# Kernel tuning notes

Measured on AMD Instinct MI355X. Metric: run time of the kernel, lower is better.

The kernel has to match this reference:

```python
import jax, jax.numpy as jnp
import numpy as np

NUM_HEADS = 4
KEY_DIM = 8
WINDOW = 4
SHIFT = 2
CHANNELS = 32


def setup_inputs() -> dict:
    key = jax.random.key(0)
    ks = jax.random.split(key, 9)
    C, H, D = CHANNELS, NUM_HEADS, KEY_DIM
    s = 0.05
    return {
        "x": jax.random.normal(ks[0], (4, 512, 512, C), jnp.float32),
        "Wq": jax.random.normal(ks[1], (C, H, D), jnp.float32) * s,
        "bq": jax.random.normal(ks[2], (H, D), jnp.float32) * s,
        "Wk": jax.random.normal(ks[3], (C, H, D), jnp.float32) * s,
        "bk": jax.random.normal(ks[4], (H, D), jnp.float32) * s,
        "Wv": jax.random.normal(ks[5], (C, H, D), jnp.float32) * s,
        "bv": jax.random.normal(ks[6], (H, D), jnp.float32) * s,
        "Wo": jax.random.normal(ks[7], (H, D, C), jnp.float32) * s,
        "bo": jax.random.normal(ks[8], (C,), jnp.float32) * s,
    }


def reference(x, Wq, bq, Wk, bk, Wv, bv, Wo, bo):
    B, H, W, C = x.shape
    ws, sh = WINDOW, SHIFT
    pad_h = (ws - H % ws) % ws
    pad_w = (ws - W % ws) % ws
    p = jnp.pad(x, ((0, 0), (0, pad_h), (0, pad_w), (0, 0)))
    if sh:
        p = jnp.roll(p, shift=(-sh, -sh), axis=(1, 2))
    Hp, Wp = H + pad_h, W + pad_w
    hw, ww = Hp // ws, Wp // ws
    # partition into windows: [B*hw*ww, ws*ws, C]
    win = p.reshape(B, hw, ws, ww, ws, C).transpose(0, 1, 3, 2, 4, 5)
    win = win.reshape(-1, ws * ws, C)
    # multi-head self-attention within each window (Keras MultiHeadAttention math)
    q = jnp.einsum('bnc,chd->bnhd', win, Wq) + bq
    k = jnp.einsum('bnc,chd->bnhd', win, Wk) + bk
    v = jnp.einsum('bnc,chd->bnhd', win, Wv) + bv
    scores = jnp.einsum('bqhd,bkhd->bhqk', q, k) / np.sqrt(KEY_DIM).astype(np.float32)
    attn = jax.nn.softmax(scores, axis=-1)
    o = jnp.einsum('bhqk,bkhd->bqhd', attn, v)
    out = jnp.einsum('bqhd,hdc->bqc', o, Wo) + bo
    # merge windows back: [B, Hp, Wp, C]
    out = out.reshape(B, hw, ww, ws, ws, C).transpose(0, 1, 3, 2, 4, 5)
    out = out.reshape(B, Hp, Wp, C)
    if sh:
        out = jnp.roll(out, shift=(sh, sh), axis=(1, 2))
    out = out[:, :H, :W, :]
    return x + out
```

## Files before the change

kernel.cpp:

```cpp
#include <hip/hip_runtime.h>
#include <hip/hip_bf16.h>
#include <stdint.h>

typedef float f32x4 __attribute__((ext_vector_type(4)));
typedef short s16x8 __attribute__((ext_vector_type(8)));
typedef unsigned short u16;
typedef u16 u16x4 __attribute__((ext_vector_type(4)));

__device__ __forceinline__ u16 f2bf(float f) {
    union { __hip_bfloat16 h; u16 u; } cv;
    cv.h = __float2bfloat16(f);
    return cv.u;
}
__device__ __forceinline__ f32x4 mfma16(s16x8 a, s16x8 b, f32x4 c) {
    return __builtin_amdgcn_mfma_f32_16x16x32_bf16(a, b, c, 0, 0, 0);
}
__device__ __forceinline__ float exp2_hw(float x) {
    float r; asm("v_exp_f32 %0, %1" : "=v"(r) : "v"(x)); return r;
}
#define LDS_FENCE() asm volatile("s_waitcnt lgkmcnt(0)" ::: "memory")

__global__ __launch_bounds__(256) void swin_attn_kernel(
    const float* __restrict__ x,
    const float* __restrict__ Wq, const float* __restrict__ bq,
    const float* __restrict__ Wk, const float* __restrict__ bk,
    const float* __restrict__ Wv, const float* __restrict__ bv,
    const float* __restrict__ Wo, const float* __restrict__ bo,
    float* __restrict__ out)
{
    const int lane  = threadIdx.x & 63;
    const int wave  = threadIdx.x >> 6;
    const int col16 = lane & 15;
    const int g     = lane >> 4;

    __shared__ __align__(16) u16 qk_bf[4][16][72];
    __shared__ __align__(16) u16 vT_bf[4][32][24];
    __shared__ __align__(16) u16 p_bf[4][4][16][24];
    __shared__ __align__(16) u16 o_bf[4][16][40];

    const float scale  = 0.35355339059327373f;
    const float qscale = scale * 1.4426950408889634f;

    s16x8 wqkv[6];
    #pragma unroll
    for (int j = 0; j < 6; ++j) {
        const float* Wsrc = (j < 2) ? Wq : (j < 4) ? Wk : Wv;
        const int colW = ((j & 1) << 4) | col16;
        const float sc = (j < 2) ? qscale : 1.0f;
        s16x8 wf;
        #pragma unroll
        for (int jj = 0; jj < 8; ++jj)
            wf[jj] = (short)f2bf(Wsrc[(g * 8 + jj) * 32 + colW] * sc);
        wqkv[j] = wf;
    }
    f32x4 bias_qk[4];
    #pragma unroll
    for (int j = 0; j < 4; ++j) {
        const float* bsrc = (j < 2) ? bq : bk;
        const float sc = (j < 2) ? qscale : 1.0f;
        #pragma unroll
        for (int i = 0; i < 4; ++i)
            bias_qk[j][i] = bsrc[((j & 1) << 4) + 4 * g + i] * sc;
    }
    f32x4 bias_v[2];
    #pragma unroll
    for (int jv = 0; jv < 2; ++jv) {
        float b = bv[jv * 16 + col16];
        bias_v[jv] = (f32x4){b, b, b, b};
    }
    s16x8 wo_frag[2];
    f32x4 bo_frag[2];
    #pragma unroll
    for (int j2 = 0; j2 < 2; ++j2) {
        const int cout = j2 * 16 + col16;
        s16x8 wf;
        #pragma unroll
        for (int jj = 0; jj < 8; ++jj)
            wf[jj] = (short)f2bf(Wo[(g * 8 + jj) * 32 + cout]);
        wo_frag[j2] = wf;
        #pragma unroll
        for (int i = 0; i < 4; ++i)
            bo_frag[j2][i] = bo[j2 * 16 + 4 * g + i];
    }

    const f32x4 zero4 = {0.f, 0.f, 0.f, 0.f};
    const s16x8 zero8 = {0, 0, 0, 0, 0, 0, 0, 0};

    const int wbase = (blockIdx.x * 4 + wave) * 4;
    long curpix;
    f32x4 px0, px1;
    {
        const int w = wbase;
        const int b = w >> 14, rem = w & 16383, wi = rem >> 7, wj = rem & 127;
        const int row  = (wi * 4 + (col16 >> 2) + 2) & 511;
        const int colp = (wj * 4 + (col16 & 3) + 2) & 511;
        curpix = ((((long)b << 9) + row) * 512 + colp) * 32;
        px0 = *(const f32x4*)(x + curpix + g * 8);
        px1 = *(const f32x4*)(x + curpix + g * 8 + 4);
    }

    #pragma unroll 1
    for (int it = 0; it < 4; ++it) {
        s16x8 xfrag;
        #pragma unroll
        for (int i = 0; i < 4; ++i) {
            xfrag[i]     = (short)f2bf(px0[i]);
            xfrag[i + 4] = (short)f2bf(px1[i]);
        }
        const long pixbase = curpix;

        #pragma unroll
        for (int j = 0; j < 4; ++j) {
            f32x4 c = mfma16(wqkv[j], xfrag, bias_qk[j]);
            u16x4 qv;
            #pragma unroll
            for (int i = 0; i < 4; ++i) qv[i] = f2bf(c[i]);
            *(u16x4*)&qk_bf[wave][col16][j * 16 + 4 * g] = qv;
        }
        #pragma unroll
        for (int jv = 0; jv < 2; ++jv) {
            f32x4 c = mfma16(xfrag, wqkv[4 + jv], bias_v[jv]);
            u16x4 vv;
            #pragma unroll
            for (int i = 0; i < 4; ++i) vv[i] = f2bf(c[i]);
            *(u16x4*)&vT_bf[wave][jv * 16 + col16][4 * g] = vv;
        }

        {
            const int w = wbase + ((it + 1) & 3);
            const int b = w >> 14, rem = w & 16383, wi = rem >> 7, wj = rem & 127;
            const int row  = (wi * 4 + (col16 >> 2) + 2) & 511;
            const int colp = (wj * 4 + (col16 & 3) + 2) & 511;
            const long np = ((((long)b << 9) + row) * 512 + colp) * 32;
            px0 = *(const f32x4*)(x + np + g * 8);
            px1 = *(const f32x4*)(x + np + g * 8 + 4);
            curpix = np;
        }
        f32x4 r0 = *(const f32x4*)(x + pixbase + 4 * g);
        f32x4 r1 = *(const f32x4*)(x + pixbase + 16 + 4 * g);

        LDS_FENCE();

        f32x4 s[4];
        #pragma unroll
        for (int h = 0; h < 4; ++h) {
            s16x8 afrag = zero8, bfrag = zero8;
            if (g == 0) {
                afrag = *(const s16x8*)&qk_bf[wave][col16][32 + h * 8];
                bfrag = *(const s16x8*)&qk_bf[wave][col16][h * 8];
            }
            s[h] = mfma16(afrag, bfrag, zero4);
        }
        #pragma unroll
        for (int h = 0; h < 4; ++h) {
            float p0 = exp2_hw(s[h][0]);
            float p1 = exp2_hw(s[h][1]);
            float p2 = exp2_hw(s[h][2]);
            float p3 = exp2_hw(s[h][3]);
            float sum = (p0 + p1) + (p2 + p3);
            sum += __shfl_xor(sum, 16);
            sum += __shfl_xor(sum, 32);
            const float inv = __builtin_amdgcn_rcpf(sum);
            u16x4 pv;
            pv[0] = f2bf(p0 * inv); pv[1] = f2bf(p1 * inv);
            pv[2] = f2bf(p2 * inv); pv[3] = f2bf(p3 * inv);
            *(u16x4*)&p_bf[wave][h][col16][4 * g] = pv;
        }
        LDS_FENCE();

        #pragma unroll
        for (int h = 0; h < 4; ++h) {
            s16x8 vfrag = zero8, pfrag = zero8;
            if (g < 2) {
                vfrag = *(const s16x8*)&vT_bf[wave][h * 8 + (col16 & 7)][g * 8];
                pfrag = *(const s16x8*)&p_bf[wave][h][col16][g * 8];
            }
            f32x4 oc = mfma16(vfrag, pfrag, zero4);
            if (g < 2) {
                u16x4 ov;
                #pragma unroll
                for (int i = 0; i < 4; ++i) ov[i] = f2bf(oc[i]);
                *(u16x4*)&o_bf[wave][col16][h * 8 + 4 * g] = ov;
            }
        }
        LDS_FENCE();

        s16x8 ofrag = *(const s16x8*)&o_bf[wave][col16][g * 8];
        {
            f32x4 c = mfma16(wo_frag[0], ofrag, bo_frag[0]);
            #pragma unroll
            for (int i = 0; i < 4; ++i) c[i] += r0[i];
            *(f32x4*)(out + pixbase + 4 * g) = c;
        }
        {
            f32x4 c = mfma16(wo_frag[1], ofrag, bo_frag[1]);
            #pragma unroll
            for (int i = 0; i < 4; ++i) c[i] += r1[i];
            *(f32x4*)(out + pixbase + 16 + 4 * g) = c;
        }
    }
}

extern "C" void kernel_launch(void* const* d_in, const int* in_sizes, int n_in,
                              void* d_out, int out_size, void* d_ws, size_t ws_size,
                              hipStream_t stream) {
    const float* x  = (const float*)d_in[0];
    const float* Wq = (const float*)d_in[1];
    const float* bq = (const float*)d_in[2];
    const float* Wk = (const float*)d_in[3];
    const float* bk = (const float*)d_in[4];
    const float* Wv = (const float*)d_in[5];
    const float* bv = (const float*)d_in[6];
    const float* Wo = (const float*)d_in[7];
    const float* bo = (const float*)d_in[8];
    float* out = (float*)d_out;

    dim3 grid(4096), block(256);
    hipLaunchKernelGGL(swin_attn_kernel, grid, block, 0, stream,
                       x, Wq, bq, Wk, bk, Wv, bv, Wo, bo, out);
}
```

Before: 64.65 us.

## Keep attention fragments in registers using 32x32 MFMA and cross-lane permutes

Removes all LDS staging of Q/K/V, probabilities and outputs. Fragments are now exchanged through permlane32_swap and ds_swizzle, and head pairs are batched into 32x32x16 MFMAs with weight layouts permuted to match. The aim is to remove the LDS round-trips and waitcnt stalls between stages. In exchange it adds block-diagonal masking work, more register pressure, and a launch-bounds occupancy hint.

```diff
diff --git a/kernel.cpp b/kernel.cpp
--- a/kernel.cpp
+++ b/kernel.cpp
@@ -3,24 +3,46 @@
 #include <stdint.h>
 
 typedef float f32x4 __attribute__((ext_vector_type(4)));
+typedef float f32x16 __attribute__((ext_vector_type(16)));
 typedef short s16x8 __attribute__((ext_vector_type(8)));
 typedef unsigned short u16;
-typedef u16 u16x4 __attribute__((ext_vector_type(4)));
 
 __device__ __forceinline__ u16 f2bf(float f) {
     union { __hip_bfloat16 h; u16 u; } cv;
     cv.h = __float2bfloat16(f);
     return cv.u;
 }
+__device__ __forceinline__ int pkbf(float lo, float hi) {
+    return (int)(unsigned)f2bf(lo) | ((int)(unsigned)f2bf(hi) << 16);
+}
 __device__ __forceinline__ f32x4 mfma16(s16x8 a, s16x8 b, f32x4 c) {
     return __builtin_amdgcn_mfma_f32_16x16x32_bf16(a, b, c, 0, 0, 0);
 }
+__device__ __forceinline__ f32x16 mfma32(s16x8 a, s16x8 b, f32x16 c) {
+    return __builtin_amdgcn_mfma_f32_32x32x16_bf16(a, b, c, 0, 0, 0);
+}
 __device__ __forceinline__ float exp2_hw(float x) {
     float r; asm("v_exp_f32 %0, %1" : "=v"(r) : "v"(x)); return r;
 }
-#define LDS_FENCE() asm volatile("s_waitcnt lgkmcnt(0)" ::: "memory")
-
-__global__ __launch_bounds__(256) void swin_attn_kernel(
+__device__ __forceinline__ int swz16(int v) {
+    return __builtin_amdgcn_ds_swizzle(v, 0x401F);
+}
+__device__ __forceinline__ int pl_hi_to_lo(int v) {
+    auto r = __builtin_amdgcn_permlane32_swap(v, v, false, false);
+    return r[1];
+}
+__device__ __forceinline__ void pl_pair(int a, int b, int* xo, int* yo) {
+    auto r = __builtin_amdgcn_permlane32_swap(a, b, false, false);
+    *xo = r[0];
+    *yo = r[1];
+}
+__device__ __forceinline__ s16x8 frag4(int d0, int d1, int d2, int d3) {
+    union { int i[4]; s16x8 v; } u;
+    u.i[0] = d0; u.i[1] = d1; u.i[2] = d2; u.i[3] = d3;
+    return u.v;
+}
+
+__global__ __launch_bounds__(256, 3) void swin_attn_kernel(
     const float* __restrict__ x,
     const float* __restrict__ Wq, const float* __restrict__ bq,
     const float* __restrict__ Wk, const float* __restrict__ bk,
@@ -28,30 +50,36 @@
     const float* __restrict__ Wo, const float* __restrict__ bo,
     float* __restrict__ out)
 {
-    const int lane  = threadIdx.x & 63;
-    const int wave  = threadIdx.x >> 6;
-    const int col16 = lane & 15;
-    const int g     = lane >> 4;
-
-    __shared__ __align__(16) u16 qk_bf[4][16][72];
-    __shared__ __align__(16) u16 vT_bf[4][32][24];
-    __shared__ __align__(16) u16 p_bf[4][4][16][24];
-    __shared__ __align__(16) u16 o_bf[4][16][40];
-
-    const float scale  = 0.35355339059327373f;
-    const float qscale = scale * 1.4426950408889634f;
+    const int lane = threadIdx.x & 63;
+    const int wave = threadIdx.x >> 6;
+    const int c16  = lane & 15;
+    const int g    = lane >> 4;
+    const int hc   = g & 1;
+    const bool lo32  = (lane < 32);
+    const bool rowok = (hc == 0);
+
+    const float qscale = 0.35355339059327373f * 1.4426950408889634f;
 
     s16x8 wqkv[6];
     #pragma unroll
-    for (int j = 0; j < 6; ++j) {
-        const float* Wsrc = (j < 2) ? Wq : (j < 4) ? Wk : Wv;
-        const int colW = ((j & 1) << 4) | col16;
+    for (int j = 0; j < 4; ++j) {
+        const float* Wsrc = (j < 2) ? Wq : Wk;
         const float sc = (j < 2) ? qscale : 1.0f;
+        const int h = c16 >> 2, d = (j & 1) * 4 + (c16 & 3);
         s16x8 wf;
         #pragma unroll
         for (int jj = 0; jj < 8; ++jj)
-            wf[jj] = (short)f2bf(Wsrc[(g * 8 + jj) * 32 + colW] * sc);
+            wf[jj] = (short)f2bf(Wsrc[(g * 8 + jj) * 32 + h * 8 + d] * sc);
         wqkv[j] = wf;
+    }
+    #pragma unroll
+    for (int jv = 0; jv < 2; ++jv) {
+        const int h = jv * 2 + (c16 >> 3), d = c16 & 7;
+        s16x8 wf;
+        #pragma unroll
+        for (int jj = 0; jj < 8; ++jj)
+            wf[jj] = (short)f2bf(Wv[(g * 8 + jj) * 32 + h * 8 + d]);
+        wqkv[4 + jv] = wf;
     }
     f32x4 bias_qk[4];
     #pragma unroll
@@ -60,31 +88,56 @@
         const float sc = (j < 2) ? qscale : 1.0f;
         #pragma unroll
         for (int i = 0; i < 4; ++i)
-            bias_qk[j][i] = bsrc[((j & 1) << 4) + 4 * g + i] * sc;
+            bias_qk[j][i] = bsrc[g * 8 + (j & 1) * 4 + i] * sc;
     }
     f32x4 bias_v[2];
     #pragma unroll
     for (int jv = 0; jv < 2; ++jv) {
-        float b = bv[jv * 16 + col16];
+        float b = bv[(jv * 2 + (c16 >> 3)) * 8 + (c16 & 7)];
         bias_v[jv] = (f32x4){b, b, b, b};
     }
     s16x8 wo_frag[2];
     f32x4 bo_frag[2];
     #pragma unroll
     for (int j2 = 0; j2 < 2; ++j2) {
-        const int cout = j2 * 16 + col16;
+        const int cout = j2 * 16 + c16;
         s16x8 wf;
         #pragma unroll
-        for (int jj = 0; jj < 8; ++jj)
-            wf[jj] = (short)f2bf(Wo[(g * 8 + jj) * 32 + cout]);
+        for (int jj = 0; jj < 8; ++jj) {
+            const int h = (g & 1) + 2 * (jj >> 2);
+            const int d = 4 * (g >> 1) + (jj & 3);
+            wf[jj] = (short)f2bf(Wo[(h * 8 + d) * 32 + cout]);
+        }
         wo_frag[j2] = wf;
         #pragma unroll
         for (int i = 0; i < 4; ++i)
             bo_frag[j2][i] = bo[j2 * 16 + 4 * g + i];
     }
 
-    const f32x4 zero4 = {0.f, 0.f, 0.f, 0.f};
-    const s16x8 zero8 = {0, 0, 0, 0, 0, 0, 0, 0};
+    f32x16 zero16;
+    #pragma unroll
+    for (int i = 0; i < 16; ++i) zero16[i] = 0.0f;
+
+    auto softmax_pack = [&](const f32x16& S) -> s16x8 {
+        float e[8];
+        #pragma unroll
+        for (int i = 0; i < 8; ++i) {
+            float sv = hc ? S[8 + i] : S[i];
+            e[i] = exp2_hw(sv);
+        }
+        float s = ((e[0] + e[1]) + (e[2] + e[3])) + ((e[4] + e[5]) + (e[6] + e[7]));
+        auto rs = __builtin_amdgcn_permlane32_swap(__float_as_int(s), __float_as_int(s), false, false);
+        float partner = lo32 ? __int_as_float(rs[1]) : __int_as_float(rs[0]);
+        float inv = __builtin_amdgcn_rcpf(s + partner);
+        #pragma unroll
+        for (int i = 0; i < 8; ++i) e[i] *= inv;
+        int dw0 = pkbf(e[0], e[1]), dw1 = pkbf(e[2], e[3]);
+        int dw2 = pkbf(e[4], e[5]), dw3 = pkbf(e[6], e[7]);
+        int a0, b0, a1, b1;
+        pl_pair(dw0, dw2, &a0, &b0);
+        pl_pair(dw1, dw3, &a1, &b1);
+        return frag4(a0, a1, b0, b1);
+    };
 
     const int wbase = (blockIdx.x * 4 + wave) * 4;
     long curpix;
@@ -92,8 +145,8 @@
     {
         const int w = wbase;
         const int b = w >> 14, rem = w & 16383, wi = rem >> 7, wj = rem & 127;
-        const int row  = (wi * 4 + (col16 >> 2) + 2) & 511;
-        const int colp = (wj * 4 + (col16 & 3) + 2) & 511;
+        const int row  = (wi * 4 + (c16 >> 2) + 2) & 511;
+        const int colp = (wj * 4 + (c16 & 3) + 2) & 511;
         curpix = ((((long)b << 9) + row) * 512 + colp) * 32;
         px0 = *(const f32x4*)(x + curpix + g * 8);
         px1 = *(const f32x4*)(x + curpix + g * 8 + 4);
@@ -101,36 +154,15 @@
 
     #pragma unroll 1
     for (int it = 0; it < 4; ++it) {
-        s16x8 xfrag;
-        #pragma unroll
-        for (int i = 0; i < 4; ++i) {
-            xfrag[i]     = (short)f2bf(px0[i]);
-            xfrag[i + 4] = (short)f2bf(px1[i]);
-        }
         const long pixbase = curpix;
-
-        #pragma unroll
-        for (int j = 0; j < 4; ++j) {
-            f32x4 c = mfma16(wqkv[j], xfrag, bias_qk[j]);
-            u16x4 qv;
-            #pragma unroll
-            for (int i = 0; i < 4; ++i) qv[i] = f2bf(c[i]);
-            *(u16x4*)&qk_bf[wave][col16][j * 16 + 4 * g] = qv;
-        }
-        #pragma unroll
-        for (int jv = 0; jv < 2; ++jv) {
-            f32x4 c = mfma16(xfrag, wqkv[4 + jv], bias_v[jv]);
-            u16x4 vv;
-            #pragma unroll
-            for (int i = 0; i < 4; ++i) vv[i] = f2bf(c[i]);
-            *(u16x4*)&vT_bf[wave][jv * 16 + col16][4 * g] = vv;
-        }
+        s16x8 xfrag = frag4(pkbf(px0[0], px0[1]), pkbf(px0[2], px0[3]),
+                            pkbf(px1[0], px1[1]), pkbf(px1[2], px1[3]));
 
         {
             const int w = wbase + ((it + 1) & 3);
             const int b = w >> 14, rem = w & 16383, wi = rem >> 7, wj = rem & 127;
-            const int row  = (wi * 4 + (col16 >> 2) + 2) & 511;
-            const int colp = (wj * 4 + (col16 & 3) + 2) & 511;
+            const int row  = (wi * 4 + (c16 >> 2) + 2) & 511;
+            const int colp = (wj * 4 + (c16 & 3) + 2) & 511;
             const long np = ((((long)b << 9) + row) * 512 + colp) * 32;
             px0 = *(const f32x4*)(x + np + g * 8);
             px1 = *(const f32x4*)(x + np + g * 8 + 4);
@@ -139,65 +171,61 @@
         f32x4 r0 = *(const f32x4*)(x + pixbase + 4 * g);
         f32x4 r1 = *(const f32x4*)(x + pixbase + 16 + 4 * g);
 
-        LDS_FENCE();
-
-        f32x4 s[4];
-        #pragma unroll
-        for (int h = 0; h < 4; ++h) {
-            s16x8 afrag = zero8, bfrag = zero8;
-            if (g == 0) {
-                afrag = *(const s16x8*)&qk_bf[wave][col16][32 + h * 8];
-                bfrag = *(const s16x8*)&qk_bf[wave][col16][h * 8];
-            }
-            s[h] = mfma16(afrag, bfrag, zero4);
-        }
-        #pragma unroll
-        for (int h = 0; h < 4; ++h) {
-            float p0 = exp2_hw(s[h][0]);
-            float p1 = exp2_hw(s[h][1]);
-            float p2 = exp2_hw(s[h][2]);
-            float p3 = exp2_hw(s[h][3]);
-            float sum = (p0 + p1) + (p2 + p3);
-            sum += __shfl_xor(sum, 16);
-            sum += __shfl_xor(sum, 32);
-            const float inv = __builtin_amdgcn_rcpf(sum);
-            u16x4 pv;
-            pv[0] = f2bf(p0 * inv); pv[1] = f2bf(p1 * inv);
-            pv[2] = f2bf(p2 * inv); pv[3] = f2bf(p3 * inv);
-            *(u16x4*)&p_bf[wave][h][col16][4 * g] = pv;
-        }
-        LDS_FENCE();
-
-        #pragma unroll
-        for (int h = 0; h < 4; ++h) {
-            s16x8 vfrag = zero8, pfrag = zero8;
-            if (g < 2) {
-                vfrag = *(const s16x8*)&vT_bf[wave][h * 8 + (col16 & 7)][g * 8];
-                pfrag = *(const s16x8*)&p_bf[wave][h][col16][g * 8];
-            }
-            f32x4 oc = mfma16(vfrag, pfrag, zero4);
-            if (g < 2) {
-                u16x4 ov;
-                #pragma unroll
-                for (int i = 0; i < 4; ++i) ov[i] = f2bf(oc[i]);
-                *(u16x4*)&o_bf[wave][col16][h * 8 + 4 * g] = ov;
-            }
-        }
-        LDS_FENCE();
-
-        s16x8 ofrag = *(const s16x8*)&o_bf[wave][col16][g * 8];
-        {
-            f32x4 c = mfma16(wo_frag[0], ofrag, bo_frag[0]);
-            #pragma unroll
-            for (int i = 0; i < 4; ++i) c[i] += r0[i];
-            *(f32x4*)(out + pixbase + 4 * g) = c;
-        }
-        {
-            f32x4 c = mfma16(wo_frag[1], ofrag, bo_frag[1]);
-            #pragma unroll
-            for (int i = 0; i < 4; ++i) c[i] += r1[i];
-            *(f32x4*)(out + pixbase + 16 + 4 * g) = c;
-        }
+        f32x4 cq0 = mfma16(wqkv[0], xfrag, bias_qk[0]);
+        f32x4 cq1 = mfma16(wqkv[1], xfrag, bias_qk[1]);
+        f32x4 ck0 = mfma16(wqkv[2], xfrag, bias_qk[2]);
+        f32x4 ck1 = mfma16(wqkv[3], xfrag, bias_qk[3]);
+        f32x4 cv0 = mfma16(xfrag, wqkv[4], bias_v[0]);
+        f32x4 cv1 = mfma16(xfrag, wqkv[5], bias_v[1]);
+
+        int qd0 = pkbf(cq0[0], cq0[1]), qd1 = pkbf(cq0[2], cq0[3]);
+        int qd2 = pkbf(cq1[0], cq1[1]), qd3 = pkbf(cq1[2], cq1[3]);
+        int kd0 = pkbf(ck0[0], ck0[1]), kd1 = pkbf(ck0[2], ck0[3]);
+        int kd2 = pkbf(ck1[0], ck1[1]), kd3 = pkbf(ck1[2], ck1[3]);
+        int ve0 = pkbf(cv0[0], cv0[1]), ve1 = pkbf(cv0[2], cv0[3]);
+        int vf0 = pkbf(cv1[0], cv1[1]), vf1 = pkbf(cv1[2], cv1[3]);
+
+        int ve0s = swz16(ve0), ve1s = swz16(ve1);
+        int vf0s = swz16(vf0), vf1s = swz16(vf1);
+
+        s16x8 ka1 = frag4(kd0, kd1, kd2, kd3);
+        s16x8 qb1 = frag4(lo32 ? qd0 : 0, lo32 ? qd1 : 0,
+                          lo32 ? qd2 : 0, lo32 ? qd3 : 0);
+        s16x8 ka2 = frag4(pl_hi_to_lo(kd0), pl_hi_to_lo(kd1),
+                          pl_hi_to_lo(kd2), pl_hi_to_lo(kd3));
+        int qp0 = pl_hi_to_lo(qd0), qp1 = pl_hi_to_lo(qd1);
+        int qp2 = pl_hi_to_lo(qd2), qp3 = pl_hi_to_lo(qd3);
+        s16x8 qb2 = frag4(lo32 ? qp0 : 0, lo32 ? qp1 : 0,
+                          lo32 ? qp2 : 0, lo32 ? qp3 : 0);
+
+        f32x16 S1 = mfma32(ka1, qb1, zero16);
+        f32x16 S2 = mfma32(ka2, qb2, zero16);
+
+        s16x8 pf1 = softmax_pack(S1);
+        s16x8 pf2 = softmax_pack(S2);
+
+        s16x8 va1 = frag4(rowok ? ve0 : 0, rowok ? ve1 : 0,
+                          rowok ? ve0s : 0, rowok ? ve1s : 0);
+        s16x8 va2 = frag4(rowok ? vf0 : 0, rowok ? vf1 : 0,
+                          rowok ? vf0s : 0, rowok ? vf1s : 0);
+        f32x16 O1 = mfma32(va1, pf1, zero16);
+        f32x16 O2 = mfma32(va2, pf2, zero16);
+
+        float o1[4], o2[4];
+        #pragma unroll
+        for (int i = 0; i < 4; ++i) {
+            o1[i] = hc ? O1[4 + i] : O1[i];
+            o2[i] = hc ? O2[4 + i] : O2[i];
+        }
+        s16x8 ofrag = frag4(pkbf(o1[0], o1[1]), pkbf(o1[2], o1[3]),
+                            pkbf(o2[0], o2[1]), pkbf(o2[2], o2[3]));
+        f32x4 ci0 = bo_frag[0], ci1 = bo_frag[1];
+        #pragma unroll
+        for (int i = 0; i < 4; ++i) { ci0[i] += r0[i]; ci1[i] += r1[i]; }
+        f32x4 c0 = mfma16(wo_frag[0], ofrag, ci0);
+        f32x4 c1 = mfma16(wo_frag[1], ofrag, ci1);
+        *(f32x4*)(out + pixbase + 4 * g) = c0;
+        *(f32x4*)(out + pixbase + 16 + 4 * g) = c1;
     }
 }
 
```

Result: slower. 102.0 us (+57.7%).

## Fuse per-head softmax with PV and pass attention output via permlane swaps

Applied to the files above, without the earlier changes.

Softmax and the P·V MFMA now run together per head, so the probability buffer shrinks to one head's worth of LDS. The O tile no longer round-trips through LDS: it is packed to bf16 and moved between lane halves with permlane32_swap. The row-sum reduction uses ds_swizzle plus a permlane swap instead of shuffles, and the residual is folded into the output MFMA accumulator. Explicit lgkmcnt waits become compiler-only fences, which relies on in-order LDS access within a wave. The kernel likely stays memory-bound, which limits what these instruction savings can change.

```diff
diff --git a/kernel.cpp b/kernel.cpp
--- a/kernel.cpp
+++ b/kernel.cpp
@@ -12,13 +12,32 @@
     cv.h = __float2bfloat16(f);
     return cv.u;
 }
+__device__ __forceinline__ int pkbf(float lo, float hi) {
+    return (int)(unsigned)f2bf(lo) | ((int)(unsigned)f2bf(hi) << 16);
+}
 __device__ __forceinline__ f32x4 mfma16(s16x8 a, s16x8 b, f32x4 c) {
     return __builtin_amdgcn_mfma_f32_16x16x32_bf16(a, b, c, 0, 0, 0);
 }
 __device__ __forceinline__ float exp2_hw(float x) {
     float r; asm("v_exp_f32 %0, %1" : "=v"(r) : "v"(x)); return r;
 }
-#define LDS_FENCE() asm volatile("s_waitcnt lgkmcnt(0)" ::: "memory")
+__device__ __forceinline__ int swz16(int v) {
+    return __builtin_amdgcn_ds_swizzle(v, 0x401F);
+}
+__device__ __forceinline__ int pl_lo_to_hi(int v) {
+    auto r = __builtin_amdgcn_permlane32_swap(v, v, false, false);
+    return r[0];
+}
+__device__ __forceinline__ float xor32_other(float v, bool lo32) {
+    auto r = __builtin_amdgcn_permlane32_swap(__float_as_int(v), __float_as_int(v), false, false);
+    return lo32 ? __int_as_float(r[1]) : __int_as_float(r[0]);
+}
+__device__ __forceinline__ s16x8 frag4(int d0, int d1, int d2, int d3) {
+    union { int i[4]; s16x8 v; } u;
+    u.i[0] = d0; u.i[1] = d1; u.i[2] = d2; u.i[3] = d3;
+    return u.v;
+}
+#define C_FENCE() asm volatile("" ::: "memory")
 
 __global__ __launch_bounds__(256) void swin_attn_kernel(
     const float* __restrict__ x,
@@ -30,22 +49,21 @@
 {
     const int lane  = threadIdx.x & 63;
     const int wave  = threadIdx.x >> 6;
-    const int col16 = lane & 15;
+    const int c16   = lane & 15;
     const int g     = lane >> 4;
+    const bool lo32 = (lane < 32);
 
     __shared__ __align__(16) u16 qk_bf[4][16][72];
     __shared__ __align__(16) u16 vT_bf[4][32][24];
-    __shared__ __align__(16) u16 p_bf[4][4][16][24];
-    __shared__ __align__(16) u16 o_bf[4][16][40];
-
-    const float scale  = 0.35355339059327373f;
-    const float qscale = scale * 1.4426950408889634f;
+    __shared__ __align__(16) u16 p_bf[4][16][24];
+
+    const float qscale = 0.35355339059327373f * 1.4426950408889634f;
 
     s16x8 wqkv[6];
     #pragma unroll
     for (int j = 0; j < 6; ++j) {
         const float* Wsrc = (j < 2) ? Wq : (j < 4) ? Wk : Wv;
-        const int colW = ((j & 1) << 4) | col16;
+        const int colW = ((j & 1) << 4) | c16;
         const float sc = (j < 2) ? qscale : 1.0f;
         s16x8 wf;
         #pragma unroll
@@ -65,18 +83,21 @@
     f32x4 bias_v[2];
     #pragma unroll
     for (int jv = 0; jv < 2; ++jv) {
-        float b = bv[jv * 16 + col16];
+        float b = bv[jv * 16 + c16];
         bias_v[jv] = (f32x4){b, b, b, b};
     }
     s16x8 wo_frag[2];
     f32x4 bo_frag[2];
     #pragma unroll
     for (int j2 = 0; j2 < 2; ++j2) {
-        const int cout = j2 * 16 + col16;
+        const int cout = j2 * 16 + c16;
         s16x8 wf;
         #pragma unroll
-        for (int jj = 0; jj < 8; ++jj)
-            wf[jj] = (short)f2bf(Wo[(g * 8 + jj) * 32 + cout]);
+        for (int jj = 0; jj < 8; ++jj) {
+            const int h = (g >> 1) * 2 + (jj >> 2);
+            const int d = 4 * (g & 1) + (jj & 3);
+            wf[jj] = (short)f2bf(Wo[(h * 8 + d) * 32 + cout]);
+        }
         wo_frag[j2] = wf;
         #pragma unroll
         for (int i = 0; i < 4; ++i)
@@ -92,8 +113,8 @@
     {
         const int w = wbase;
         const int b = w >> 14, rem = w & 16383, wi = rem >> 7, wj = rem & 127;
-        const int row  = (wi * 4 + (col16 >> 2) + 2) & 511;
-        const int colp = (wj * 4 + (col16 & 3) + 2) & 511;
+        const int row  = (wi * 4 + (c16 >> 2) + 2) & 511;
+        const int colp = (wj * 4 + (c16 & 3) + 2) & 511;
         curpix = ((((long)b << 9) + row) * 512 + colp) * 32;
         px0 = *(const f32x4*)(x + curpix + g * 8);
         px1 = *(const f32x4*)(x + curpix + g * 8 + 4);
@@ -101,13 +122,9 @@
 
     #pragma unroll 1
     for (int it = 0; it < 4; ++it) {
-        s16x8 xfrag;
-        #pragma unroll
-        for (int i = 0; i < 4; ++i) {
-            xfrag[i]     = (short)f2bf(px0[i]);
-            xfrag[i + 4] = (short)f2bf(px1[i]);
-        }
         const long pixbase = curpix;
+        s16x8 xfrag = frag4(pkbf(px0[0], px0[1]), pkbf(px0[2], px0[3]),
+                            pkbf(px1[0], px1[1]), pkbf(px1[2], px1[3]));
 
         #pragma unroll
         for (int j = 0; j < 4; ++j) {
@@ -115,7 +132,7 @@
             u16x4 qv;
             #pragma unroll
             for (int i = 0; i < 4; ++i) qv[i] = f2bf(c[i]);
-            *(u16x4*)&qk_bf[wave][col16][j * 16 + 4 * g] = qv;
+            *(u16x4*)&qk_bf[wave][c16][j * 16 + 4 * g] = qv;
         }
         #pragma unroll
         for (int jv = 0; jv < 2; ++jv) {
@@ -123,14 +140,14 @@
             u16x4 vv;
             #pragma unroll
             for (int i = 0; i < 4; ++i) vv[i] = f2bf(c[i]);
-            *(u16x4*)&vT_bf[wave][jv * 16 + col16][4 * g] = vv;
+            *(u16x4*)&vT_bf[wave][jv * 16 + c16][4 * g] = vv;
         }
 
         {
             const int w = wbase + ((it + 1) & 3);
             const int b = w >> 14, rem = w & 16383, wi = rem >> 7, wj = rem & 127;
-            const int row  = (wi * 4 + (col16 >> 2) + 2) & 511;
-            const int colp = (wj * 4 + (col16 & 3) + 2) & 511;
+            const int row  = (wi * 4 + (c16 >> 2) + 2) & 511;
+            const int colp = (wj * 4 + (c16 & 3) + 2) & 511;
             const long np = ((((long)b << 9) + row) * 512 + colp) * 32;
             px0 = *(const f32x4*)(x + np + g * 8);
             px1 = *(const f32x4*)(x + np + g * 8 + 4);
@@ -139,65 +156,57 @@
         f32x4 r0 = *(const f32x4*)(x + pixbase + 4 * g);
         f32x4 r1 = *(const f32x4*)(x + pixbase + 16 + 4 * g);
 
-        LDS_FENCE();
-
-        f32x4 s[4];
+        C_FENCE();
+
+        f32x4 o_acc[4];
         #pragma unroll
         for (int h = 0; h < 4; ++h) {
             s16x8 afrag = zero8, bfrag = zero8;
             if (g == 0) {
-                afrag = *(const s16x8*)&qk_bf[wave][col16][32 + h * 8];
-                bfrag = *(const s16x8*)&qk_bf[wave][col16][h * 8];
+                afrag = *(const s16x8*)&qk_bf[wave][c16][32 + h * 8];
+                bfrag = *(const s16x8*)&qk_bf[wave][c16][h * 8];
             }
-            s[h] = mfma16(afrag, bfrag, zero4);
-        }
-        #pragma unroll
-        for (int h = 0; h < 4; ++h) {
-            float p0 = exp2_hw(s[h][0]);
-            float p1 = exp2_hw(s[h][1]);
-            float p2 = exp2_hw(s[h][2]);
-            float p3 = exp2_hw(s[h][3]);
-            float sum = (p0 + p1) + (p2 + p3);
-            sum += __shfl_xor(sum, 16);
-            sum += __shfl_xor(sum, 32);
+            f32x4 s = mfma16(afrag, bfrag, zero4);
+
+            float e0 = exp2_hw(s[0]), e1 = exp2_hw(s[1]);
+            float e2 = exp2_hw(s[2]), e3 = exp2_hw(s[3]);
+            float part = (e0 + e1) + (e2 + e3);
+            float sum  = part + __int_as_float(swz16(__float_as_int(part)));
+            sum += xor32_other(sum, lo32);
             const float inv = __builtin_amdgcn_rcpf(sum);
             u16x4 pv;
-            pv[0] = f2bf(p0 * inv); pv[1] = f2bf(p1 * inv);
-            pv[2] = f2bf(p2 * inv); pv[3] = f2bf(p3 * inv);
-            *(u16x4*)&p_bf[wave][h][col16][4 * g] = pv;
-        }
-        LDS_FENCE();
-
-        #pragma unroll
-        for (int h = 0; h < 4; ++h) {
+            pv[0] = f2bf(e0 * inv); pv[1] = f2bf(e1 * inv);
+            pv[2] = f2bf(e2 * inv); pv[3] = f2bf(e3 * inv);
+            *(u16x4*)&p_bf[wave][c16][4 * g] = pv;
+            C_FENCE();
+
             s16x8 vfrag = zero8, pfrag = zero8;
             if (g < 2) {
-                vfrag = *(const s16x8*)&vT_bf[wave][h * 8 + (col16 & 7)][g * 8];
-                pfrag = *(const s16x8*)&p_bf[wave][h][col16][g * 8];
+                vfrag = *(const s16x8*)&vT_bf[wave][h * 8 + (c16 & 7)][g * 8];
+                pfrag = *(const s16x8*)&p_bf[wave][c16][g * 8];
             }
-            f32x4 oc = mfma16(vfrag, pfrag, zero4);
-            if (g < 2) {
-                u16x4 ov;
-                #pragma unroll
-                for (int i = 0; i < 4; ++i) ov[i] = f2bf(oc[i]);
-                *(u16x4*)&o_bf[wave][col16][h * 8 + 4 * g] = ov;
-            }
-        }
-        LDS_FENCE();
-
-        s16x8 ofrag = *(const s16x8*)&o_bf[wave][col16][g * 8];
-        {
-            f32x4 c = mfma16(wo_frag[0], ofrag, bo_frag[0]);
-            #pragma unroll
-            for (int i = 0; i < 4; ++i) c[i] += r0[i];
-            *(f32x4*)(out + pixbase + 4 * g) = c;
-        }
-        {
-            f32x4 c = mfma16(wo_frag[1], ofrag, bo_frag[1]);
-            #pragma unroll
-            for (int i = 0; i < 4; ++i) c[i] += r1[i];
-            *(f32x4*)(out + pixbase + 16 + 4 * g) = c;
-        }
+            o_acc[h] = mfma16(vfrag, pfrag, zero4);
+            C_FENCE();
+        }
+
+        int t00 = pkbf(o_acc[0][0], o_acc[0][1]), t01 = pkbf(o_acc[0][2], o_acc[0][3]);
+        int t10 = pkbf(o_acc[1][0], o_acc[1][1]), t11 = pkbf(o_acc[1][2], o_acc[1][3]);
+        int t20 = pkbf(o_acc[2][0], o_acc[2][1]), t21 = pkbf(o_acc[2][2], o_acc[2][3]);
+        int t30 = pkbf(o_acc[3][0], o_acc[3][1]), t31 = pkbf(o_acc[3][2], o_acc[3][3]);
+        int m20 = pl_lo_to_hi(t20), m21 = pl_lo_to_hi(t21);
+        int m30 = pl_lo_to_hi(t30), m31 = pl_lo_to_hi(t31);
+        s16x8 ofrag = frag4(lo32 ? t00 : m20, lo32 ? t01 : m21,
+                            lo32 ? t10 : m30, lo32 ? t11 : m31);
+
+        f32x4 ci0 = bo_frag[0], ci1 = bo_frag[1];
+        #pragma unroll
+        for (int i = 0; i < 4; ++i) { ci0[i] += r0[i]; ci1[i] += r1[i]; }
+        f32x4 c0 = mfma16(wo_frag[0], ofrag, ci0);
+        f32x4 c1 = mfma16(wo_frag[1], ofrag, ci1);
+        *(f32x4*)(out + pixbase + 4 * g) = c0;
+        *(f32x4*)(out + pixbase + 16 + 4 * g) = c1;
+
+        C_FENCE();
     }
 }
 
```

Result: slower. 66.90 us (+3.5%).
